# Optimization experiments

Hardware: AMD Instinct MI355X
Metric: run time of the kernel (lower is better)

## Reference

```python
import jax, jax.numpy as jnp
import numpy as np
from jax import lax

B0, C0, H0, W0 = 4, 128, 48, 48
GR = 32  # growth rate
NL = 4   # dense layers


def conv1x1(x, w, b):
    # w: [O, Cin], x: [B, Cin, H, W]
    return jnp.einsum('oc,bchw->bohw', w, x) + b[None, :, None, None]


def conv3x3(x, w, b):
    y = lax.conv_general_dilated(x, w, (1, 1), [(1, 1), (1, 1)],
                                 dimension_numbers=('NCHW', 'OIHW', 'NCHW'))
    return y + b[None, :, None, None]


def batchnorm(x, g, b, eps=1e-5):
    # training-mode BatchNorm2d: batch statistics over (B, H, W)
    mu = jnp.mean(x, axis=(0, 2, 3), keepdims=True)
    var = jnp.var(x, axis=(0, 2, 3), keepdims=True)
    return (x - mu) * lax.rsqrt(var + eps) * g[None, :, None, None] + b[None, :, None, None]


def apply_rope(x):
    B, C, H, W = x.shape
    half = C // 2
    theta = 1.0 / (10000.0 ** (jnp.arange(half, dtype=x.dtype) / half))
    # pos_emb[h, w, j] = (h + w) * theta[j]
    pos = (jnp.arange(H, dtype=x.dtype)[:, None, None]
           + jnp.arange(W, dtype=x.dtype)[None, :, None]) * theta
    cos = jnp.cos(pos).transpose(2, 0, 1)  # [half, H, W]
    sin = jnp.sin(pos).transpose(2, 0, 1)
    xr = x.reshape(B, half, 2, H, W)
    x_re, x_im = xr[:, :, 0], xr[:, :, 1]
    rr = x_re * cos - x_im * sin
    ri = x_re * sin + x_im * cos
    return jnp.stack([rr, ri], axis=2).reshape(B, C, H, W)


def setup_inputs() -> dict:
    key = jax.random.key(0)
    ks = iter(jax.random.split(key, 64))
    def nrm(shape, s=0.05):
        return jax.random.normal(next(ks), shape, jnp.float32) * s
    C = C0
    dc = C + NL * GR  # 256 dense-block output channels
    hid = 4 * C
    d = {
        'x': jax.random.normal(next(ks), (B0, C0, H0, W0), jnp.float32),
        'r_w': nrm((C, C)), 'r_b': jnp.zeros((C,), jnp.float32),
        'k_w': nrm((C, C)), 'k_b': jnp.zeros((C,), jnp.float32),
        'v_w': nrm((C, C)), 'v_b': jnp.zeros((C,), jnp.float32),
        'wc1_w': nrm((C // 4, C, 3, 3)), 'wc1_b': jnp.zeros((C // 4,), jnp.float32),
        'wc2_w': nrm((C, C // 4)), 'wc2_b': jnp.zeros((C,), jnp.float32),
        'u': nrm((C,), 0.1),
        'sn1_w': nrm((dc // 4, dc)), 'sn1_b': jnp.zeros((dc // 4,), jnp.float32),
        'sn2_w': nrm((dc, dc // 4)), 'sn2_b': jnp.zeros((dc,), jnp.float32),
        'lb_w': nrm((C // 4, dc)), 'lb_b': jnp.zeros((C // 4,), jnp.float32),
        'ld_w': nrm((C // 4, dc)), 'ld_b': jnp.zeros((C // 4,), jnp.float32),
        'ps_w': nrm((C, C // 4)), 'ps_b': jnp.zeros((C,), jnp.float32),
        'pq_w': nrm((C, C)), 'pq_b': jnp.zeros((C,), jnp.float32),
        'fc1_w': nrm((hid, C)), 'fc1_b': jnp.zeros((hid,), jnp.float32),
        'fc2_w': nrm((C, hid)), 'fc2_b': jnp.zeros((C,), jnp.float32),
    }
    for i in range(NL):
        cin = C + i * GR
        d[f'db_g{i}'] = jnp.ones((cin,), jnp.float32)
        d[f'db_b{i}'] = jnp.zeros((cin,), jnp.float32)
        d[f'db_w{i}'] = nrm((GR, cin, 3, 3))
        d[f'db_cb{i}'] = jnp.zeros((GR,), jnp.float32)
    return d


def _forward(x, r_w, r_b, k_w, k_b, v_w, v_b, wc1_w, wc1_b, wc2_w, wc2_b, u,
             db_g0, db_b0, db_w0, db_cb0, db_g1, db_b1, db_w1, db_cb1,
             db_g2, db_b2, db_w2, db_cb2, db_g3, db_b3, db_w3, db_cb3,
             sn1_w, sn1_b, sn2_w, sn2_b, lb_w, lb_b, ld_w, ld_b,
             ps_w, ps_b, pq_w, pq_b, fc1_w, fc1_b, fc2_w, fc2_b):
    B, C, H, W = x.shape
    N = H * W
    # decay gate w (hidden is None so it multiplies zeros, kept for fidelity)
    w_gate = jax.nn.sigmoid(conv1x1(jax.nn.relu(conv3x3(x, wc1_w, wc1_b)), wc2_w, wc2_b)).reshape(B, C, N)
    x_rope = apply_rope(x)
    r = jax.nn.sigmoid(conv1x1(x, r_w, r_b))
    k = conv1x1(x_rope, k_w, k_b).reshape(B, C, N)
    v = conv1x1(x_rope, v_w, v_b).reshape(B, C, N)
    zeros = jnp.zeros_like(k)
    new_num = zeros * jnp.exp(-w_gate) + k * v
    new_den = zeros * jnp.exp(-w_gate) + k
    eu = jnp.exp(u)[None, :, None]
    wkv = ((new_num + eu * k * v) / (new_den + eu * k)).reshape(B, C, H, W)
    recursive_output = r * wkv
    # dense block (concat-growth)
    feats = x
    for g, bb, wt, cb in ((db_g0, db_b0, db_w0, db_cb0), (db_g1, db_b1, db_w1, db_cb1),
                          (db_g2, db_b2, db_w2, db_cb2), (db_g3, db_b3, db_w3, db_cb3)):
        h = jax.nn.relu(batchnorm(feats, g, bb))
        feats = jnp.concatenate([feats, conv3x3(h, wt, cb)], axis=1)
    df = feats  # [B, C+4*GR, H, W]
    # adaptive spiking neuron
    tau = jnp.mean(jax.nn.sigmoid(conv1x1(jax.nn.relu(conv1x1(df, sn1_w, sn1_b)), sn2_w, sn2_b)),
                   axis=(2, 3), keepdims=True)
    spike_prob = jax.nn.sigmoid((df - 1.0) * 5.0)
    sf = spike_prob * (df * jnp.exp(-1.0 / (tau + 1e-6))) + (1.0 - spike_prob) * df
    # first attention over N tokens, channels = C//4
    Bf = conv1x1(sf, lb_w, lb_b).reshape(B, -1, N)
    Df = conv1x1(sf, ld_w, ld_b).reshape(B, -1, N)
    attn = jax.nn.softmax(jnp.einsum('bcn,bcm->bnm', Bf, Bf), axis=-1)
    att1 = jnp.einsum('bnm,bcm->bcn', attn, Df).reshape(B, -1, H, W)
    spike_output = conv1x1(att1, ps_w, ps_b)
    combined = recursive_output + spike_output
    # second attention (k/v convs are shared with WKV path)
    Q = conv1x1(combined, pq_w, pq_b).reshape(B, C, N)
    K = conv1x1(combined, k_w, k_b).reshape(B, C, N)
    V = conv1x1(combined, v_w, v_b).reshape(B, C, N)
    scores = jnp.einsum('bcn,bcm->bnm', Q, K) / jnp.sqrt(jnp.asarray(C, x.dtype))
    aw = jax.nn.softmax(scores, axis=-1)
    att2 = jnp.einsum('bnm,bcm->bcn', aw, V).reshape(B, C, H, W)
    x1 = x + att2
    out = x1 + conv1x1(jax.nn.relu(conv1x1(x1, fc1_w, fc1_b)) ** 2, fc2_w, fc2_b)
    return out, new_num, new_den


def reference(x, r_w, r_b, k_w, k_b, v_w, v_b, wc1_w, wc1_b, wc2_w, wc2_b, u,
              db_g0, db_b0, db_w0, db_cb0, db_g1, db_b1, db_w1, db_cb1,
              db_g2, db_b2, db_w2, db_cb2, db_g3, db_b3, db_w3, db_cb3,
              sn1_w, sn1_b, sn2_w, sn2_b, lb_w, lb_b, ld_w, ld_b,
              ps_w, ps_b, pq_w, pq_b, fc1_w, fc1_b, fc2_w, fc2_b):
    return _forward(x, r_w, r_b, k_w, k_b, v_w, v_b, wc1_w, wc1_b, wc2_w, wc2_b, u,
                    db_g0, db_b0, db_w0, db_cb0, db_g1, db_b1, db_w1, db_cb1,
                    db_g2, db_b2, db_w2, db_cb2, db_g3, db_b3, db_w3, db_cb3,
                    sn1_w, sn1_b, sn2_w, sn2_b, lb_w, lb_b, ld_w, ld_b,
                    ps_w, ps_b, pq_w, pq_b, fc1_w, fc1_b, fc2_w, fc2_b)
```

## Files before the change

kernel.cpp:

```cpp
#include <hip/hip_runtime.h>
#include <math.h>

#define BB 4
#define CC 128
#define HH 48
#define WW 48
#define NSP (HH*WW)
#define DCC 256
#define BCN (BB*CC*NSP)
#define KS 4

typedef float f32x4 __attribute__((ext_vector_type(4)));
typedef __bf16 bf16x8 __attribute__((ext_vector_type(8)));
typedef __bf16 bf16x4 __attribute__((ext_vector_type(4)));

__device__ __forceinline__ float sigmf(float v) { return 1.0f / (1.0f + __expf(-v)); }

struct Prep {
  const float* wsrc[13];
  int wlen[13];
  int woff[13];
  const float* psrc[4];
  int pcin[4];
  int poff[4];
  const float* x;
  float* sums;
  float* sums2;
  __bf16* x_t;
  __bf16* xrope_t;
};
__global__ __launch_bounds__(256) void prep_kernel(Prep a, __bf16* __restrict__ wdst,
                                                   __bf16* __restrict__ pdst) {
  __shared__ float lds[32][33];
  __shared__ float rs[4], rs2[4];
  int g = blockIdx.y;
  int idx = blockIdx.x * 256 + threadIdx.x;
  if (g < 13) {
    if (idx < a.wlen[g]) wdst[a.woff[g] + idx] = (__bf16)a.wsrc[g][idx];
  } else if (g < 17) {
    int L = g - 13;
    int cin = a.pcin[L];
    if (idx < 9 * 32 * cin) {
      int c = idx % cin;
      int o = (idx / cin) % 32;
      int tap = idx / (cin * 32);
      pdst[a.poff[L] + idx] = (__bf16)a.psrc[L][((size_t)o * cin + c) * 9 + tap];
    }
  } else if (g == 17) {
    int c = blockIdx.x;
    if (c >= 128) return;
    float s = 0.f, s2 = 0.f;
    for (int i = threadIdx.x; i < BB * NSP; i += 256) {
      int b = i / NSP, n = i % NSP;
      float v = a.x[((size_t)b * 128 + c) * NSP + n];
      s += v;
      s2 += v * v;
    }
#pragma unroll
    for (int off = 32; off > 0; off >>= 1) {
      s += __shfl_down(s, off);
      s2 += __shfl_down(s2, off);
    }
    int wid = threadIdx.x >> 6;
    if ((threadIdx.x & 63) == 0) { rs[wid] = s; rs2[wid] = s2; }
    __syncthreads();
    if (threadIdx.x == 0) {
      a.sums[c] = rs[0] + rs[1] + rs[2] + rs[3];
      a.sums2[c] = rs2[0] + rs2[1] + rs2[2] + rs2[3];
    }
  } else {
    int T = (g - 18) * 256 + blockIdx.x;
    if (T >= 1152) return;
    int b = T / 288;
    int r = T % 288;
    int c0 = (r / 72) * 32;
    int n0 = (r % 72) * 32;
    int tid = threadIdx.x;
    int nn = tid & 31, cs = tid >> 5;
#pragma unroll
    for (int j = 0; j < 4; ++j) {
      int cc = c0 + cs * 4 + j;
      lds[cs * 4 + j][nn] = a.x[((size_t)b * 128 + cc) * NSP + n0 + nn];
    }
    __syncthreads();
    int c = tid & 31, ns = tid >> 5;
#pragma unroll
    for (int j = 0; j < 4; ++j) {
      int n2 = ns * 4 + j;
      float pv = lds[c][n2];
      a.x_t[((size_t)b * NSP + n0 + n2) * 128 + c0 + c] = (__bf16)pv;
      int gc = c0 + c;
      int i = gc >> 1;
      float re = lds[c & ~1][n2];
      float im = lds[c | 1][n2];
      int n = n0 + n2;
      int h = n / WW, w = n % WW;
      float theta = __expf(-9.2103403719761836f * ((float)i) / 64.0f);
      float pos = (float)(h + w) * theta;
      float cs_ = cosf(pos), sn_ = sinf(pos);
      float vr_ = (gc & 1) ? (re * sn_ + im * cs_) : (re * cs_ - im * sn_);
      a.xrope_t[((size_t)b * NSP + n0 + n2) * 128 + c0 + c] = (__bf16)vr_;
    }
  }
}

__global__ __launch_bounds__(256) void kvr_kernel(
    const __bf16* __restrict__ xrope_t, const __bf16* __restrict__ x_t,
    const __bf16* __restrict__ wk, const __bf16* __restrict__ wvp,
    const __bf16* __restrict__ wr,
    const float* __restrict__ k_b, const float* __restrict__ v_b,
    const float* __restrict__ r_b, const float* __restrict__ u,
    float* __restrict__ kden, float* __restrict__ knum, float* __restrict__ rec) {
  int tid = threadIdx.x;
  int wv = tid >> 6, lane = tid & 63;
  int m15 = lane & 15, quad = lane >> 4;
  int b = blockIdx.y;
  int n0 = blockIdx.x * 16;
  int o0 = wv * 32;
  int n = n0 + m15;
  const __bf16* brr = xrope_t + ((size_t)b * NSP + n) * 128 + quad * 8;
  const __bf16* brx = x_t + ((size_t)b * NSP + n) * 128 + quad * 8;
  const __bf16* ak0 = wk + (size_t)(o0 + m15) * 128 + quad * 8;
  const __bf16* ak1 = wk + (size_t)(o0 + 16 + m15) * 128 + quad * 8;
  const __bf16* av0 = wvp + (size_t)(o0 + m15) * 128 + quad * 8;
  const __bf16* av1 = wvp + (size_t)(o0 + 16 + m15) * 128 + quad * 8;
  const __bf16* ar0 = wr + (size_t)(o0 + m15) * 128 + quad * 8;
  const __bf16* ar1 = wr + (size_t)(o0 + 16 + m15) * 128 + quad * 8;
  f32x4 fk[2], fv[2], fr[2];
#pragma unroll
  for (int t = 0; t < 2; ++t) {
    fk[t] = (f32x4){0.f, 0.f, 0.f, 0.f};
    fv[t] = (f32x4){0.f, 0.f, 0.f, 0.f};
    fr[t] = (f32x4){0.f, 0.f, 0.f, 0.f};
  }
#pragma unroll
  for (int kc = 0; kc < 128; kc += 32) {
    bf16x8 br_ = *(const bf16x8*)(brr + kc);
    bf16x8 bx_ = *(const bf16x8*)(brx + kc);
    fk[0] = __builtin_amdgcn_mfma_f32_16x16x32_bf16(*(const bf16x8*)(ak0 + kc), br_, fk[0], 0, 0, 0);
    fk[1] = __builtin_amdgcn_mfma_f32_16x16x32_bf16(*(const bf16x8*)(ak1 + kc), br_, fk[1], 0, 0, 0);
    fv[0] = __builtin_amdgcn_mfma_f32_16x16x32_bf16(*(const bf16x8*)(av0 + kc), br_, fv[0], 0, 0, 0);
    fv[1] = __builtin_amdgcn_mfma_f32_16x16x32_bf16(*(const bf16x8*)(av1 + kc), br_, fv[1], 0, 0, 0);
    fr[0] = __builtin_amdgcn_mfma_f32_16x16x32_bf16(*(const bf16x8*)(ar0 + kc), bx_, fr[0], 0, 0, 0);
    fr[1] = __builtin_amdgcn_mfma_f32_16x16x32_bf16(*(const bf16x8*)(ar1 + kc), bx_, fr[1], 0, 0, 0);
  }
#pragma unroll
  for (int t = 0; t < 2; ++t) {
#pragma unroll
    for (int reg = 0; reg < 4; ++reg) {
      int ol = o0 + t * 16 + quad * 4 + reg;
      float kk = fk[t][reg] + k_b[ol];
      float vv = fv[t][reg] + v_b[ol];
      float rr = sigmf(fr[t][reg] + r_b[ol]);
      float eu = __expf(u[ol]);
      size_t idx = ((size_t)b * 128 + ol) * NSP + n;
      float nv = kk * vv, tt = eu * kk;
      kden[idx] = kk;
      knum[idx] = nv;
      rec[idx] = rr * ((nv + tt * vv) / (kk + tt));
    }
  }
}

template <int OUT>
__device__ __forceinline__ void gemm_store(void* outp, int b, int n, int Oseg,
                                           int obase, int quad, const float* vr) {
  if (OUT == 0) {
    float* op = (float*)outp;
#pragma unroll
    for (int reg = 0; reg < 4; ++reg)
      op[((size_t)b * Oseg + obase + quad * 4 + reg) * NSP + n] = vr[reg];
  } else if (OUT == 1) {
    __bf16* op = (__bf16*)outp;
    bf16x4 pk;
#pragma unroll
    for (int reg = 0; reg < 4; ++reg) pk[reg] = (__bf16)vr[reg];
    *(bf16x4*)(op + ((size_t)b * NSP + n) * Oseg + obase + quad * 4) = pk;
  } else {
    __bf16* op = (__bf16*)outp;
#pragma unroll
    for (int reg = 0; reg < 4; ++reg)
      op[((size_t)b * Oseg + obase + quad * 4 + reg) * NSP + n] = (__bf16)vr[reg];
  }
}

template <int K, int ACT, int OUT0, int OUT1, int OUT2, int SPLITB>
__global__ __launch_bounds__(256) void gemm_mfma_kernel(
    const __bf16* __restrict__ in_t, const __bf16* __restrict__ in_t2,
    const __bf16* __restrict__ wb,
    const float* __restrict__ bias0, const float* __restrict__ bias1,
    const float* __restrict__ bias2,
    const float* __restrict__ add0, const float* __restrict__ add1,
    void* __restrict__ out0, void* __restrict__ out1, void* __restrict__ out2,
    int osplit, int osplit2, int Ototal, float sc0, float sc1, float sc2) {
  int tid = threadIdx.x;
  int wv = tid >> 6, lane = tid & 63;
  int m15 = lane & 15, quad = lane >> 4;
  int b = blockIdx.y;
  int n0 = blockIdx.x * 16;
  int wpb = blockDim.x >> 6;
  int o0 = (blockIdx.z * wpb + wv) * 32;
  if (o0 >= Ototal) return;
  int n = n0 + m15;
  const __bf16* brow = in_t + ((size_t)b * NSP + n) * (SPLITB ? 128 : K) + quad * 8;
  const __bf16* brow2 = SPLITB ? (in_t2 + ((size_t)b * NSP + n) * 128 + quad * 8) : nullptr;
  const __bf16* a0p = wb + (size_t)(o0 + m15) * K + quad * 8;
  const __bf16* a1p = wb + (size_t)(o0 + 16 + m15) * K + quad * 8;
  f32x4 of0 = (f32x4){0.f, 0.f, 0.f, 0.f};
  f32x4 of1 = (f32x4){0.f, 0.f, 0.f, 0.f};
#pragma unroll
  for (int kc = 0; kc < K; kc += 32) {
    bf16x8 bfr;
    if constexpr (SPLITB) {
      bfr = (kc < 128) ? *(const bf16x8*)(brow + kc) : *(const bf16x8*)(brow2 + (kc - 128));
    } else {
      bfr = *(const bf16x8*)(brow + kc);
    }
    bf16x8 a0 = *(const bf16x8*)(a0p + kc);
    bf16x8 a1 = *(const bf16x8*)(a1p + kc);
    of0 = __builtin_amdgcn_mfma_f32_16x16x32_bf16(a0, bfr, of0, 0, 0, 0);
    of1 = __builtin_amdgcn_mfma_f32_16x16x32_bf16(a1, bfr, of1, 0, 0, 0);
  }
  int seg = (o0 >= osplit2) ? 2 : (o0 >= osplit) ? 1 : 0;
  int segb = (seg == 2) ? osplit2 : (seg == 1) ? osplit : 0;
  int sege = (seg == 2) ? Ototal : (seg == 1) ? osplit2 : osplit;
  int Oseg = sege - segb;
  int ol0 = o0 - segb;
  const float* bias = (seg == 2) ? bias2 : (seg == 1) ? bias1 : bias0;
  const float* add = (seg == 2) ? nullptr : (seg == 1) ? add1 : add0;
  void* outp = (seg == 2) ? out2 : (seg == 1) ? out1 : out0;
  float sc = (seg == 2) ? sc2 : (seg == 1) ? sc1 : sc0;
#pragma unroll
  for (int t = 0; t < 2; ++t) {
    f32x4 acc = t ? of1 : of0;
    float vr[4];
#pragma unroll
    for (int reg = 0; reg < 4; ++reg) {
      int ol = ol0 + t * 16 + quad * 4 + reg;
      float v = acc[reg] + bias[ol];
      if (ACT == 1) v = fmaxf(v, 0.0f);
      else if (ACT == 2) v = sigmf(v);
      else if (ACT == 3) { v = fmaxf(v, 0.0f); v = v * v; }
      v *= sc;
      if (add) v += add[((size_t)b * Oseg + ol) * NSP + n];
      vr[reg] = v;
    }
    if (seg == 0) gemm_store<OUT0>(outp, b, n, Oseg, ol0 + t * 16, quad, vr);
    else if (seg == 1) gemm_store<OUT1>(outp, b, n, Oseg, ol0 + t * 16, quad, vr);
    else gemm_store<OUT2>(outp, b, n, Oseg, ol0 + t * 16, quad, vr);
  }
}

__global__ __launch_bounds__(256) void sn12_kernel(
    const __bf16* __restrict__ x_t, const __bf16* __restrict__ dense_t,
    const __bf16* __restrict__ wsn1, const float* __restrict__ sn1_b,
    const __bf16* __restrict__ wsn2, const float* __restrict__ sn2_b,
    float* __restrict__ taupart) {
  __shared__ __bf16 z1l[16][72];
  int tid = threadIdx.x;
  int wv = tid >> 6, lane = tid & 63;
  int m15 = lane & 15, quad = lane >> 4;
  int b = blockIdx.y;
  int n0 = blockIdx.x * 16;
  int n = n0 + m15;
  if (wv < 2) {
    int o0 = wv * 32;
    const __bf16* bx = x_t + ((size_t)b * NSP + n) * 128 + quad * 8;
    const __bf16* bd = dense_t + ((size_t)b * NSP + n) * 128 + quad * 8;
    const __bf16* a0p = wsn1 + (size_t)(o0 + m15) * 256 + quad * 8;
    const __bf16* a1p = wsn1 + (size_t)(o0 + 16 + m15) * 256 + quad * 8;
    f32x4 of0 = (f32x4){0.f, 0.f, 0.f, 0.f};
    f32x4 of1 = (f32x4){0.f, 0.f, 0.f, 0.f};
#pragma unroll
    for (int kc = 0; kc < 256; kc += 32) {
      bf16x8 bfr = (kc < 128) ? *(const bf16x8*)(bx + kc) : *(const bf16x8*)(bd + (kc - 128));
      bf16x8 a0 = *(const bf16x8*)(a0p + kc);
      bf16x8 a1 = *(const bf16x8*)(a1p + kc);
      of0 = __builtin_amdgcn_mfma_f32_16x16x32_bf16(a0, bfr, of0, 0, 0, 0);
      of1 = __builtin_amdgcn_mfma_f32_16x16x32_bf16(a1, bfr, of1, 0, 0, 0);
    }
#pragma unroll
    for (int t = 0; t < 2; ++t) {
      f32x4 acc = t ? of1 : of0;
#pragma unroll
      for (int reg = 0; reg < 4; ++reg) {
        int ol = o0 + t * 16 + quad * 4 + reg;
        z1l[m15][ol] = (__bf16)fmaxf(acc[reg] + sn1_b[ol], 0.0f);
      }
    }
  }
  __syncthreads();
  bf16x8 bfr0 = *(const bf16x8*)&z1l[m15][quad * 8];
  bf16x8 bfr1 = *(const bf16x8*)&z1l[m15][32 + quad * 8];
#pragma unroll
  for (int ot = 0; ot < 2; ++ot) {
    int o0 = (wv * 2 + ot) * 32;
    const __bf16* a0p = wsn2 + (size_t)(o0 + m15) * 64 + quad * 8;
    const __bf16* a1p = wsn2 + (size_t)(o0 + 16 + m15) * 64 + quad * 8;
    f32x4 of0 = (f32x4){0.f, 0.f, 0.f, 0.f};
    f32x4 of1 = (f32x4){0.f, 0.f, 0.f, 0.f};
    of0 = __builtin_amdgcn_mfma_f32_16x16x32_bf16(*(const bf16x8*)(a0p), bfr0, of0, 0, 0, 0);
    of0 = __builtin_amdgcn_mfma_f32_16x16x32_bf16(*(const bf16x8*)(a0p + 32), bfr1, of0, 0, 0, 0);
    of1 = __builtin_amdgcn_mfma_f32_16x16x32_bf16(*(const bf16x8*)(a1p), bfr0, of1, 0, 0, 0);
    of1 = __builtin_amdgcn_mfma_f32_16x16x32_bf16(*(const bf16x8*)(a1p + 32), bfr1, of1, 0, 0, 0);
#pragma unroll
    for (int t = 0; t < 2; ++t) {
      f32x4 acc = t ? of1 : of0;
#pragma unroll
      for (int reg = 0; reg < 4; ++reg) {
        int ol = o0 + t * 16 + quad * 4 + reg;
        float sv = sigmf(acc[reg] + sn2_b[ol]);
        sv += __shfl_xor(sv, 1);
        sv += __shfl_xor(sv, 2);
        sv += __shfl_xor(sv, 4);
        sv += __shfl_xor(sv, 8);
        if (m15 == 0)
          taupart[((size_t)(b * DCC + ol)) * 144 + blockIdx.x] = sv;
      }
    }
  }
}

__global__ __launch_bounds__(128) void lbld_sf_kernel(
    const __bf16* __restrict__ x_t, const __bf16* __restrict__ dense_t,
    const float* __restrict__ taupart, const __bf16* __restrict__ wlb,
    const float* __restrict__ lb_b, const float* __restrict__ ld_b,
    __bf16* __restrict__ Bft, __bf16* __restrict__ Dfb) {
  __shared__ float ef[256];
  int tid = threadIdx.x;
  int b = blockIdx.y;
  for (int ch = tid; ch < 256; ch += 128) {
    const f32x4* tp = (const f32x4*)(taupart + ((size_t)(b * DCC + ch)) * 144);
    f32x4 s4 = (f32x4){0.f, 0.f, 0.f, 0.f};
#pragma unroll
    for (int j = 0; j < 36; ++j) s4 += tp[j];
    float tv = (s4.x + s4.y + s4.z + s4.w) * (1.0f / (float)NSP);
    ef[ch] = __expf(-1.0f / (tv + 1e-6f)) - 1.0f;
  }
  __syncthreads();
  int wv = tid >> 6, lane = tid & 63;
  int m15 = lane & 15, quad = lane >> 4;
  int n0 = blockIdx.x * 16;
  int o0 = wv * 32;
  int n = n0 + m15;
  const __bf16* bx = x_t + ((size_t)b * NSP + n) * 128 + quad * 8;
  const __bf16* bd = dense_t + ((size_t)b * NSP + n) * 128 + quad * 8;
  const __bf16* a0p = wlb + (size_t)(o0 + m15) * 256 + quad * 8;
  const __bf16* a1p = wlb + (size_t)(o0 + 16 + m15) * 256 + quad * 8;
  f32x4 of0 = (f32x4){0.f, 0.f, 0.f, 0.f};
  f32x4 of1 = (f32x4){0.f, 0.f, 0.f, 0.f};
#pragma unroll
  for (int kc = 0; kc < 256; kc += 32) {
    bf16x8 raw = (kc < 128) ? *(const bf16x8*)(bx + kc) : *(const bf16x8*)(bd + (kc - 128));
    bf16x8 sfv;
#pragma unroll
    for (int j = 0; j < 8; ++j) {
      float df = (float)raw[j];
      float sp = sigmf((df - 1.0f) * 5.0f);
      sfv[j] = (__bf16)(df * (1.0f + sp * ef[kc + quad * 8 + j]));
    }
    bf16x8 a0 = *(const bf16x8*)(a0p + kc);
    bf16x8 a1 = *(const bf16x8*)(a1p + kc);
    of0 = __builtin_amdgcn_mfma_f32_16x16x32_bf16(a0, sfv, of0, 0, 0, 0);
    of1 = __builtin_amdgcn_mfma_f32_16x16x32_bf16(a1, sfv, of1, 0, 0, 0);
  }
  if (o0 == 0) {
#pragma unroll
    for (int t = 0; t < 2; ++t) {
      f32x4 acc = t ? of1 : of0;
      bf16x4 pk;
#pragma unroll
      for (int reg = 0; reg < 4; ++reg) pk[reg] = (__bf16)(acc[reg] + lb_b[t * 16 + quad * 4 + reg]);
      *(bf16x4*)(Bft + ((size_t)b * NSP + n) * 32 + t * 16 + quad * 4) = pk;
    }
  } else {
#pragma unroll
    for (int t = 0; t < 2; ++t) {
      f32x4 acc = t ? of1 : of0;
#pragma unroll
      for (int reg = 0; reg < 4; ++reg) {
        int ol = t * 16 + quad * 4 + reg;
        Dfb[((size_t)b * 32 + ol) * NSP + n] = (__bf16)(acc[reg] + ld_b[ol]);
      }
    }
  }
}

template <int Cin>
__global__ __launch_bounds__(256) void convbn_kernel(
    const __bf16* __restrict__ x_t, const __bf16* __restrict__ dense_t,
    const __bf16* __restrict__ wb, const float* __restrict__ cb,
    float* __restrict__ sums, float* __restrict__ sums2,
    const float* __restrict__ cpart_in,
    const float* __restrict__ g, const float* __restrict__ bbp,
    __bf16* __restrict__ dense_out, float* __restrict__ cpart_out, int cout0) {
  constexpr int KCin = Cin / 32;
  constexpr int NIT = 9 * KCin;
  __shared__ float red[4][64][8];
  __shared__ float scsh[2][Cin];
  __shared__ float tred[64][4];
  __shared__ float fin[64];
  int tid = threadIdx.x;
  const float inv = 1.0f / (float)(BB * NSP);

  if (cpart_in) {
    int row = tid >> 2, sl = tid & 3;
    const f32x4* cp = (const f32x4*)(cpart_in + (size_t)row * 576 + sl * 144);
    f32x4 s4 = (f32x4){0.f, 0.f, 0.f, 0.f};
#pragma unroll
    for (int j = 0; j < 36; ++j) s4 += cp[j];
    tred[row][sl] = s4.x + s4.y + s4.z + s4.w;
    __syncthreads();
    if (tid < 64) fin[tid] = tred[tid][0] + tred[tid][1] + tred[tid][2] + tred[tid][3];
    __syncthreads();
    if (blockIdx.x == 0 && blockIdx.y == 0 && tid < 32) {
      sums[Cin - 32 + tid] = fin[tid];
      sums2[Cin - 32 + tid] = fin[32 + tid];
    }
  }
  for (int ch = tid; ch < Cin; ch += 256) {
    float S, S2;
    if (cpart_in && ch >= Cin - 32) {
      S = fin[ch - (Cin - 32)];
      S2 = fin[ch - (Cin - 32) + 32];
    } else {
      S = sums[ch];
      S2 = sums2[ch];
    }
    float m = S * inv;
    float var = S2 * inv - m * m;
    float sc_ = rsqrtf(var + 1e-5f) * g[ch];
    scsh[0][ch] = sc_;
    scsh[1][ch] = bbp[ch] - m * sc_;
  }
  __syncthreads();

  int wv = tid >> 6, lane = tid & 63;
  int m15 = lane & 15, quad = lane >> 4;
  int b = blockIdx.y;
  int n0 = blockIdx.x * 16;
  int n = n0 + m15;
  int h = n / WW, w = n % WW;
  f32x4 of0 = (f32x4){0.f, 0.f, 0.f, 0.f};
  f32x4 of1 = (f32x4){0.f, 0.f, 0.f, 0.f};
  const __bf16* bx_ = x_t + (size_t)b * NSP * 128;
  const __bf16* bd_ = dense_t + (size_t)b * NSP * 128;
  const bf16x8 zf = {};
  int begin = (wv * NIT) / 4, end = ((wv + 1) * NIT) / 4;
  int cur = -1;
  float bsc[8], bsh[8];
  const __bf16* base = nullptr;
  for (int ci = begin; ci < end; ++ci) {
    int chunk = ci / 9;
    int tap = ci - chunk * 9;
    int kc = chunk * 32;
    if (chunk != cur) {
      cur = chunk;
      int cc = kc + quad * 8;
#pragma unroll
      for (int j = 0; j < 8; ++j) {
        bsc[j] = scsh[0][cc + j];
        bsh[j] = scsh[1][cc + j];
      }
      base = (cc < 128) ? (bx_ + cc) : (bd_ + cc - 128);
    }
    int dh = tap / 3 - 1, dw = tap % 3 - 1;
    bool valid = ((unsigned)(h + dh) < HH) && ((unsigned)(w + dw) < WW);
    int pa = valid ? (n + dh * WW + dw) : 0;
    bf16x8 raw = *(const bf16x8*)(base + (size_t)pa * 128);
    bf16x8 bfr;
#pragma unroll
    for (int j = 0; j < 8; ++j) {
      float v = fmaxf((float)raw[j] * bsc[j] + bsh[j], 0.0f);
      bfr[j] = (__bf16)v;
    }
    if (!valid) bfr = zf;
    const __bf16* wt = wb + (size_t)tap * 32 * Cin + kc + quad * 8;
    bf16x8 a0 = *(const bf16x8*)(wt + (size_t)m15 * Cin);
    bf16x8 a1 = *(const bf16x8*)(wt + (size_t)(16 + m15) * Cin);
    of0 = __builtin_amdgcn_mfma_f32_16x16x32_bf16(a0, bfr, of0, 0, 0, 0);
    of1 = __builtin_amdgcn_mfma_f32_16x16x32_bf16(a1, bfr, of1, 0, 0, 0);
  }
  float* myred = red[wv][lane];
#pragma unroll
  for (int reg = 0; reg < 4; ++reg) {
    myred[reg] = of0[reg];
    myred[4 + reg] = of1[reg];
  }
  __syncthreads();
  if (wv == 0) {
    int dloc = cout0 - 128;
    __bf16* dt = dense_out + ((size_t)b * NSP + n) * 128 + dloc;
    bf16x4 pk0, pk1;
    float sv[4][4];
#pragma unroll
    for (int reg = 0; reg < 4; ++reg) {
      int o = quad * 4 + reg;
      float v0 = red[0][lane][reg] + red[1][lane][reg] + red[2][lane][reg] +
                 red[3][lane][reg] + cb[o];
      float v1 = red[0][lane][4 + reg] + red[1][lane][4 + reg] + red[2][lane][4 + reg] +
                 red[3][lane][4 + reg] + cb[16 + o];
      pk0[reg] = (__bf16)v0;
      pk1[reg] = (__bf16)v1;
      sv[reg][0] = v0;
      sv[reg][1] = v0 * v0;
      sv[reg][2] = v1;
      sv[reg][3] = v1 * v1;
    }
    *(bf16x4*)(dt + quad * 4) = pk0;
    *(bf16x4*)(dt + 16 + quad * 4) = pk1;
    if (cpart_out) {
#pragma unroll
      for (int reg = 0; reg < 4; ++reg) {
        float a0 = sv[reg][0], q0 = sv[reg][1], a1 = sv[reg][2], q1 = sv[reg][3];
#pragma unroll
        for (int mk = 1; mk < 16; mk <<= 1) {
          a0 += __shfl_xor(a0, mk);
          q0 += __shfl_xor(q0, mk);
          a1 += __shfl_xor(a1, mk);
          q1 += __shfl_xor(q1, mk);
        }
        if (m15 == 0) {
          int o = quad * 4 + reg;
          int pidx = blockIdx.y * 144 + blockIdx.x;
          cpart_out[(size_t)o * 576 + pidx] = a0;
          cpart_out[(size_t)(32 + o) * 576 + pidx] = q0;
          cpart_out[(size_t)(16 + o) * 576 + pidx] = a1;
          cpart_out[(size_t)(48 + o) * 576 + pidx] = q1;
        }
      }
    }
  }
}

template <int CD>
__global__ __launch_bounds__(256) void attn_part_kernel(
    const __bf16* __restrict__ Qt, const __bf16* __restrict__ Kt,
    const __bf16* __restrict__ Vb, __bf16* __restrict__ Op,
    float* __restrict__ lp) {
  constexpr int NC = CD / 16;
  constexpr int KC = CD / 32;
  constexpr int KEYS = NSP / KS;
  constexpr int KP = CD + 4;
  constexpr int VP = 36;
  __shared__ __bf16 kl[32][KP];
  __shared__ __bf16 vl[CD][VP];
  int tid = threadIdx.x;
  int wv = tid >> 6, lane = tid & 63;
  int m15 = lane & 15, quad = lane >> 4;
  int b = blockIdx.y, ks = blockIdx.z;
  int n0 = blockIdx.x * 64 + wv * 16;

  bf16x8 qf[KC];
  const __bf16* qrow = Qt + ((size_t)b * NSP + n0 + m15) * CD + quad * 8;
#pragma unroll
  for (int kc = 0; kc < KC; ++kc) qf[kc] = *(const bf16x8*)(qrow + kc * 32);

  f32x4 of[NC];
#pragma unroll
  for (int i = 0; i < NC; ++i) of[i] = (f32x4){0.f, 0.f, 0.f, 0.f};
  float lsum = 0.f;

  const __bf16* Kb = Kt + (size_t)b * NSP * CD;
  const __bf16* Vbb = Vb + (size_t)b * CD * NSP;

  for (int m0 = ks * KEYS; m0 < (ks + 1) * KEYS; m0 += 32) {
    __syncthreads();
    for (int i = tid; i < 32 * CD / 8; i += 256) {
      int row = i / (CD / 8);
      int cc8 = (i % (CD / 8)) * 8;
      *(bf16x8*)&kl[row][cc8] = *(const bf16x8*)(Kb + (size_t)(m0 + row) * CD + cc8);
    }
    for (int i = tid; i < CD * 4; i += 256) {
      int ch = i / 4;
      int k8 = (i % 4) * 8;
      *(bf16x8*)&vl[ch][k8] = *(const bf16x8*)(Vbb + (size_t)ch * NSP + m0 + k8);
    }
    __syncthreads();
    f32x4 s[2];
#pragma unroll
    for (int t = 0; t < 2; ++t) {
      f32x4 acc = (f32x4){0.f, 0.f, 0.f, 0.f};
#pragma unroll
      for (int kc = 0; kc < KC; ++kc) {
        bf16x8 kf = *(const bf16x8*)&kl[t * 16 + m15][kc * 32 + quad * 8];
        acc = __builtin_amdgcn_mfma_f32_16x16x32_bf16(kf, qf[kc], acc, 0, 0, 0);
      }
      s[t] = acc;
    }
    bf16x8 pf;
#pragma unroll
    for (int t = 0; t < 2; ++t) {
#pragma unroll
      for (int r = 0; r < 4; ++r) {
        float ev = __expf(s[t][r]);
        lsum += ev;
        pf[t * 4 + r] = (__bf16)ev;
      }
    }
#pragma unroll
    for (int ct = 0; ct < NC; ++ct) {
      bf16x4 va = *(const bf16x4*)&vl[ct * 16 + m15][4 * quad];
      bf16x4 vb_ = *(const bf16x4*)&vl[ct * 16 + m15][16 + 4 * quad];
      bf16x8 vf;
#pragma unroll
      for (int j = 0; j < 4; ++j) { vf[j] = va[j]; vf[4 + j] = vb_[j]; }
      of[ct] = __builtin_amdgcn_mfma_f32_16x16x32_bf16(pf, vf, of[ct], 0, 0, 0);
    }
  }

  lsum += __shfl_xor(lsum, 16);
  lsum += __shfl_xor(lsum, 32);
  float* lpb = lp + (size_t)(ks * BB + b) * NSP + n0;
  if (quad == 0) lpb[m15] = lsum;
  __bf16* Ob = Op + (size_t)(ks * BB + b) * CD * NSP;
#pragma unroll
  for (int ct = 0; ct < NC; ++ct) {
    bf16x4 pk;
#pragma unroll
    for (int reg = 0; reg < 4; ++reg) pk[reg] = (__bf16)of[ct][reg];
    *(bf16x4*)(Ob + (size_t)(ct * 16 + m15) * NSP + n0 + quad * 4) = pk;
  }
}

__global__ __launch_bounds__(256) void c32ps_kernel(
    const __bf16* __restrict__ Op, const float* __restrict__ lp,
    const __bf16* __restrict__ wps, const float* __restrict__ ps_b,
    const float* __restrict__ rec, __bf16* __restrict__ comb_t) {
  __shared__ float lds[32][33];
  int b = blockIdx.y;
  int n0 = blockIdx.x * 32;
  int tid = threadIdx.x;
  int nn = tid & 31, cs = tid >> 5;
  float ltot = 0.f;
#pragma unroll
  for (int ks = 0; ks < KS; ++ks) ltot += lp[(size_t)(ks * BB + b) * NSP + n0 + nn];
  float linv = 1.0f / ltot;
#pragma unroll
  for (int j = 0; j < 4; ++j) {
    int cc = cs * 4 + j;
    float s = 0.f;
#pragma unroll
    for (int ks = 0; ks < KS; ++ks)
      s += (float)Op[((size_t)(ks * BB + b) * 32 + cc) * NSP + n0 + nn];
    lds[cc][nn] = s * linv;
  }
  __syncthreads();
  int wv = tid >> 6, lane = tid & 63;
  int m15 = lane & 15, quad = lane >> 4;
  int o0 = wv * 32;
  bf16x8 a0 = *(const bf16x8*)(wps + (size_t)(o0 + m15) * 32 + quad * 8);
  bf16x8 a1 = *(const bf16x8*)(wps + (size_t)(o0 + 16 + m15) * 32 + quad * 8);
#pragma unroll
  for (int t2 = 0; t2 < 2; ++t2) {
    int nl = t2 * 16 + m15;
    int n = n0 + nl;
    bf16x8 bfr;
#pragma unroll
    for (int j = 0; j < 8; ++j) bfr[j] = (__bf16)lds[quad * 8 + j][nl];
    f32x4 of0 = (f32x4){0.f, 0.f, 0.f, 0.f};
    f32x4 of1 = (f32x4){0.f, 0.f, 0.f, 0.f};
    of0 = __builtin_amdgcn_mfma_f32_16x16x32_bf16(a0, bfr, of0, 0, 0, 0);
    of1 = __builtin_amdgcn_mfma_f32_16x16x32_bf16(a1, bfr, of1, 0, 0, 0);
#pragma unroll
    for (int t = 0; t < 2; ++t) {
      f32x4 acc = t ? of1 : of0;
      bf16x4 pk;
#pragma unroll
      for (int reg = 0; reg < 4; ++reg) {
        int ol = o0 + t * 16 + quad * 4 + reg;
        float v = acc[reg] + ps_b[ol] + rec[((size_t)b * 128 + ol) * NSP + n];
        pk[reg] = (__bf16)v;
      }
      *(bf16x4*)(comb_t + ((size_t)b * NSP + n) * 128 + o0 + t * 16 + quad * 4) = pk;
    }
  }
}

__global__ __launch_bounds__(256) void combine128_kernel(
    const __bf16* __restrict__ Op, const float* __restrict__ lp,
    const float* __restrict__ x, float* __restrict__ x1, __bf16* __restrict__ x1_t) {
  __shared__ float lds[32][33];
  int b = blockIdx.z;
  int n0 = blockIdx.x * 32;
  int c0 = blockIdx.y * 32;
  int tid = threadIdx.x;
  int nn = tid & 31, cs = tid >> 5;
  float ltot = 0.f;
#pragma unroll
  for (int ks = 0; ks < KS; ++ks) ltot += lp[(size_t)(ks * BB + b) * NSP + n0 + nn];
  float linv = 1.0f / ltot;
#pragma unroll
  for (int j = 0; j < 4; ++j) {
    int gc = c0 + cs * 4 + j;
    float s = 0.f;
#pragma unroll
    for (int ks = 0; ks < KS; ++ks)
      s += (float)Op[((size_t)(ks * BB + b) * CC + gc) * NSP + n0 + nn];
    float v = s * linv + x[((size_t)b * CC + gc) * NSP + n0 + nn];
    lds[cs * 4 + j][nn] = v;
    x1[((size_t)b * CC + gc) * NSP + n0 + nn] = v;
  }
  __syncthreads();
  int c = tid & 31, ns = tid >> 5;
#pragma unroll
  for (int j = 0; j < 4; ++j) {
    int n2 = ns * 4 + j;
    x1_t[((size_t)b * NSP + n0 + n2) * CC + c0 + c] = (__bf16)lds[c][n2];
  }
}

extern "C" void kernel_launch(void* const* d_in, const int* in_sizes, int n_in,
                              void* d_out, int out_size, void* d_ws, size_t ws_size,
                              hipStream_t stream) {
  const float* x = (const float*)d_in[0];
  const float* r_w = (const float*)d_in[1];
  const float* r_b = (const float*)d_in[2];
  const float* k_w = (const float*)d_in[3];
  const float* k_b = (const float*)d_in[4];
  const float* v_w = (const float*)d_in[5];
  const float* v_b = (const float*)d_in[6];
  const float* u = (const float*)d_in[11];
  const float* sn1_w = (const float*)d_in[12];
  const float* sn1_b = (const float*)d_in[13];
  const float* sn2_w = (const float*)d_in[14];
  const float* sn2_b = (const float*)d_in[15];
  const float* lb_w = (const float*)d_in[16];
  const float* lb_b = (const float*)d_in[17];
  const float* ld_w = (const float*)d_in[18];
  const float* ld_b = (const float*)d_in[19];
  const float* ps_w = (const float*)d_in[20];
  const float* ps_b = (const float*)d_in[21];
  const float* pq_w = (const float*)d_in[22];
  const float* pq_b = (const float*)d_in[23];
  const float* fc1_w = (const float*)d_in[24];
  const float* fc1_b = (const float*)d_in[25];
  const float* fc2_w = (const float*)d_in[26];
  const float* fc2_b = (const float*)d_in[27];
  const float* db_g[4] = {(const float*)d_in[28], (const float*)d_in[32],
                          (const float*)d_in[36], (const float*)d_in[40]};
  const float* db_b[4] = {(const float*)d_in[29], (const float*)d_in[33],
                          (const float*)d_in[37], (const float*)d_in[41]};
  const float* db_w[4] = {(const float*)d_in[30], (const float*)d_in[34],
                          (const float*)d_in[38], (const float*)d_in[42]};
  const float* db_cb[4] = {(const float*)d_in[31], (const float*)d_in[35],
                           (const float*)d_in[39], (const float*)d_in[43]};

  float* outp = (float*)d_out;
  float* knum = outp + BCN;
  float* kden = outp + 2 * (size_t)BCN;

  float* ws = (float*)d_ws;
  const size_t F_FEATS = 0;
  const size_t F_REC = 4718592;
  const size_t F_V = 5898240;
  const size_t F_R = 7077888;
  const size_t F_XR = 8257536;
  const size_t F_XT = 8847360;
  const size_t F_DFB = 9437184;
  const size_t F_AT1T = 9584640;
  const size_t F_CT = 9732096;
  const size_t F_LP = 10321920;
  const size_t F_WB = 10434048;
  const size_t F_WB3 = 10575360;
  const size_t F_STATS = 10676736;
  const size_t F_TAUP = 10714112;
  float* sums = ws + F_STATS;
  float* sums2 = ws + F_STATS + 256;
  float* cpart0 = ws + F_FEATS;
  float* cpart1 = cpart0 + 36864;
  float* cpart2 = cpart1 + 36864;
  float* taupart = ws + F_TAUP;
  float* lp = ws + F_LP;
  __bf16* wbase = (__bf16*)(ws + F_WB);
  __bf16* wb3 = (__bf16*)(ws + F_WB3);
  const int W_KV = 0;
  const int W_R = 32768;
  const int W_SN1 = 49152;
  const int W_SN2 = 65536;
  const int W_LBLD = 81920;
  const int W_PS = 98304;
  const int W_PQK = 102400;
  const int W_FC1 = 151552;
  const int W_FC2 = 217088;
  const int W3_OFF[4] = {0, 36864, 82944, 138240};

  dim3 blk(256);
  __bf16* xrope_t = (__bf16*)(ws + F_XR);
  __bf16* x_t = (__bf16*)(ws + F_XT);

  Prep pp;
  pp.wsrc[0] = k_w;    pp.wlen[0] = 16384; pp.woff[0] = W_KV;
  pp.wsrc[1] = v_w;    pp.wlen[1] = 16384; pp.woff[1] = W_KV + 16384;
  pp.wsrc[2] = r_w;    pp.wlen[2] = 16384; pp.woff[2] = W_R;
  pp.wsrc[3] = sn1_w;  pp.wlen[3] = 16384; pp.woff[3] = W_SN1;
  pp.wsrc[4] = sn2_w;  pp.wlen[4] = 16384; pp.woff[4] = W_SN2;
  pp.wsrc[5] = lb_w;   pp.wlen[5] = 8192;  pp.woff[5] = W_LBLD;
  pp.wsrc[6] = ld_w;   pp.wlen[6] = 8192;  pp.woff[6] = W_LBLD + 8192;
  pp.wsrc[7] = ps_w;   pp.wlen[7] = 4096;  pp.woff[7] = W_PS;
  pp.wsrc[8] = pq_w;   pp.wlen[8] = 16384; pp.woff[8] = W_PQK;
  pp.wsrc[9] = k_w;    pp.wlen[9] = 16384; pp.woff[9] = W_PQK + 16384;
  pp.wsrc[10] = v_w;   pp.wlen[10] = 16384; pp.woff[10] = W_PQK + 32768;
  pp.wsrc[11] = fc1_w; pp.wlen[11] = 65536; pp.woff[11] = W_FC1;
  pp.wsrc[12] = fc2_w; pp.wlen[12] = 65536; pp.woff[12] = W_FC2;
  for (int i = 0; i < 4; ++i) {
    pp.psrc[i] = db_w[i];
    pp.pcin[i] = 128 + 32 * i;
    pp.poff[i] = W3_OFF[i];
  }
  pp.x = x;
  pp.sums = sums;
  pp.sums2 = sums2;
  pp.x_t = x_t;
  pp.xrope_t = xrope_t;
  prep_kernel<<<dim3(256, 23), blk, 0, stream>>>(pp, wbase, wb3);

  kvr_kernel<<<dim3(144, 4), blk, 0, stream>>>(
      xrope_t, x_t, wbase + W_KV, wbase + W_KV + 16384, wbase + W_R,
      k_b, v_b, r_b, u, kden, knum, ws + F_REC);

  __bf16* dense_t = (__bf16*)(ws + F_R);
  convbn_kernel<128><<<dim3(144, 4), blk, 0, stream>>>(
      x_t, dense_t, wb3 + W3_OFF[0], db_cb[0], sums, sums2, nullptr,
      db_g[0], db_b[0], dense_t, cpart0, 128);
  convbn_kernel<160><<<dim3(144, 4), blk, 0, stream>>>(
      x_t, dense_t, wb3 + W3_OFF[1], db_cb[1], sums, sums2, cpart0,
      db_g[1], db_b[1], dense_t, cpart1, 160);
  convbn_kernel<192><<<dim3(144, 4), blk, 0, stream>>>(
      x_t, dense_t, wb3 + W3_OFF[2], db_cb[2], sums, sums2, cpart1,
      db_g[2], db_b[2], dense_t, cpart2, 192);
  convbn_kernel<224><<<dim3(144, 4), blk, 0, stream>>>(
      x_t, dense_t, wb3 + W3_OFF[3], db_cb[3], sums, sums2, cpart2,
      db_g[3], db_b[3], dense_t, nullptr, 224);

  sn12_kernel<<<dim3(144, 4), blk, 0, stream>>>(
      x_t, dense_t, wbase + W_SN1, sn1_b, wbase + W_SN2, sn2_b, taupart);
  __bf16* Bft = (__bf16*)(ws + F_CT + 294912);
  __bf16* Dfb = (__bf16*)(ws + F_DFB);
  lbld_sf_kernel<<<dim3(144, 4), dim3(128), 0, stream>>>(
      x_t, dense_t, taupart, wbase + W_LBLD, lb_b, ld_b, Bft, Dfb);
  __bf16* Opart = (__bf16*)(ws + F_FEATS);
  attn_part_kernel<32><<<dim3(36, 4, KS), blk, 0, stream>>>(Bft, Bft, Dfb, Opart, lp);
  __bf16* comb_t = (__bf16*)(ws + F_CT);
  c32ps_kernel<<<dim3(72, 4), blk, 0, stream>>>(
      Opart, lp, wbase + W_PS, ps_b, ws + F_REC, comb_t);

  __bf16* Qt = (__bf16*)(ws + F_XR);
  __bf16* K2t = (__bf16*)(ws + F_XT);
  __bf16* V2b = (__bf16*)(ws + F_V);
  gemm_mfma_kernel<128, 0, 1, 1, 2, 0><<<dim3(144, 4, 3), blk, 0, stream>>>(
      comb_t, nullptr, wbase + W_PQK, pq_b, k_b, v_b, nullptr, nullptr,
      Qt, K2t, V2b, 128, 256, 384, 0.08838834764831845f, 1.f, 1.f);
  attn_part_kernel<128><<<dim3(36, 4, KS), blk, 0, stream>>>(Qt, K2t, V2b, Opart, lp);
  float* x1 = ws + F_R;
  __bf16* x1_t = (__bf16*)(ws + F_CT);
  combine128_kernel<<<dim3(72, 4, 4), blk, 0, stream>>>(Opart, lp, x, x1, x1_t);

  __bf16* h_t = (__bf16*)(ws + F_FEATS);
  gemm_mfma_kernel<128, 3, 1, 1, 0, 0><<<dim3(144, 4, 4), blk, 0, stream>>>(
      x1_t, nullptr, wbase + W_FC1, fc1_b, fc1_b, nullptr, nullptr, nullptr,
      h_t, h_t, nullptr, 512, 512, 512, 1.f, 1.f, 1.f);
  gemm_mfma_kernel<512, 0, 0, 0, 0, 0><<<dim3(144, 4, 1), blk, 0, stream>>>(
      h_t, nullptr, wbase + W_FC2, fc2_b, fc2_b, nullptr, x1, x1,
      outp, outp, nullptr, 128, 128, 128, 1.f, 1.f, 1.f);
}
```

Before: 405.5 us.

## Fuse projection-sum with QKV GEMM and FC1/FC2 MLP into single kernels

```diff
diff --git a/kernel.cpp b/kernel.cpp
--- a/kernel.cpp
+++ b/kernel.cpp
@@ -162,95 +162,6 @@
   }
 }
 
-template <int OUT>
-__device__ __forceinline__ void gemm_store(void* outp, int b, int n, int Oseg,
-                                           int obase, int quad, const float* vr) {
-  if (OUT == 0) {
-    float* op = (float*)outp;
-#pragma unroll
-    for (int reg = 0; reg < 4; ++reg)
-      op[((size_t)b * Oseg + obase + quad * 4 + reg) * NSP + n] = vr[reg];
-  } else if (OUT == 1) {
-    __bf16* op = (__bf16*)outp;
-    bf16x4 pk;
-#pragma unroll
-    for (int reg = 0; reg < 4; ++reg) pk[reg] = (__bf16)vr[reg];
-    *(bf16x4*)(op + ((size_t)b * NSP + n) * Oseg + obase + quad * 4) = pk;
-  } else {
-    __bf16* op = (__bf16*)outp;
-#pragma unroll
-    for (int reg = 0; reg < 4; ++reg)
-      op[((size_t)b * Oseg + obase + quad * 4 + reg) * NSP + n] = (__bf16)vr[reg];
-  }
-}
-
-template <int K, int ACT, int OUT0, int OUT1, int OUT2, int SPLITB>
-__global__ __launch_bounds__(256) void gemm_mfma_kernel(
-    const __bf16* __restrict__ in_t, const __bf16* __restrict__ in_t2,
-    const __bf16* __restrict__ wb,
-    const float* __restrict__ bias0, const float* __restrict__ bias1,
-    const float* __restrict__ bias2,
-    const float* __restrict__ add0, const float* __restrict__ add1,
-    void* __restrict__ out0, void* __restrict__ out1, void* __restrict__ out2,
-    int osplit, int osplit2, int Ototal, float sc0, float sc1, float sc2) {
-  int tid = threadIdx.x;
-  int wv = tid >> 6, lane = tid & 63;
-  int m15 = lane & 15, quad = lane >> 4;
-  int b = blockIdx.y;
-  int n0 = blockIdx.x * 16;
-  int wpb = blockDim.x >> 6;
-  int o0 = (blockIdx.z * wpb + wv) * 32;
-  if (o0 >= Ototal) return;
-  int n = n0 + m15;
-  const __bf16* brow = in_t + ((size_t)b * NSP + n) * (SPLITB ? 128 : K) + quad * 8;
-  const __bf16* brow2 = SPLITB ? (in_t2 + ((size_t)b * NSP + n) * 128 + quad * 8) : nullptr;
-  const __bf16* a0p = wb + (size_t)(o0 + m15) * K + quad * 8;
-  const __bf16* a1p = wb + (size_t)(o0 + 16 + m15) * K + quad * 8;
-  f32x4 of0 = (f32x4){0.f, 0.f, 0.f, 0.f};
-  f32x4 of1 = (f32x4){0.f, 0.f, 0.f, 0.f};
-#pragma unroll
-  for (int kc = 0; kc < K; kc += 32) {
-    bf16x8 bfr;
-    if constexpr (SPLITB) {
-      bfr = (kc < 128) ? *(const bf16x8*)(brow + kc) : *(const bf16x8*)(brow2 + (kc - 128));
-    } else {
-      bfr = *(const bf16x8*)(brow + kc);
-    }
-    bf16x8 a0 = *(const bf16x8*)(a0p + kc);
-    bf16x8 a1 = *(const bf16x8*)(a1p + kc);
-    of0 = __builtin_amdgcn_mfma_f32_16x16x32_bf16(a0, bfr, of0, 0, 0, 0);
-    of1 = __builtin_amdgcn_mfma_f32_16x16x32_bf16(a1, bfr, of1, 0, 0, 0);
-  }
-  int seg = (o0 >= osplit2) ? 2 : (o0 >= osplit) ? 1 : 0;
-  int segb = (seg == 2) ? osplit2 : (seg == 1) ? osplit : 0;
-  int sege = (seg == 2) ? Ototal : (seg == 1) ? osplit2 : osplit;
-  int Oseg = sege - segb;
-  int ol0 = o0 - segb;
-  const float* bias = (seg == 2) ? bias2 : (seg == 1) ? bias1 : bias0;
-  const float* add = (seg == 2) ? nullptr : (seg == 1) ? add1 : add0;
-  void* outp = (seg == 2) ? out2 : (seg == 1) ? out1 : out0;
-  float sc = (seg == 2) ? sc2 : (seg == 1) ? sc1 : sc0;
-#pragma unroll
-  for (int t = 0; t < 2; ++t) {
-    f32x4 acc = t ? of1 : of0;
-    float vr[4];
-#pragma unroll
-    for (int reg = 0; reg < 4; ++reg) {
-      int ol = ol0 + t * 16 + quad * 4 + reg;
-      float v = acc[reg] + bias[ol];
-      if (ACT == 1) v = fmaxf(v, 0.0f);
-      else if (ACT == 2) v = sigmf(v);
-      else if (ACT == 3) { v = fmaxf(v, 0.0f); v = v * v; }
-      v *= sc;
-      if (add) v += add[((size_t)b * Oseg + ol) * NSP + n];
-      vr[reg] = v;
-    }
-    if (seg == 0) gemm_store<OUT0>(outp, b, n, Oseg, ol0 + t * 16, quad, vr);
-    else if (seg == 1) gemm_store<OUT1>(outp, b, n, Oseg, ol0 + t * 16, quad, vr);
-    else gemm_store<OUT2>(outp, b, n, Oseg, ol0 + t * 16, quad, vr);
-  }
-}
-
 __global__ __launch_bounds__(256) void sn12_kernel(
     const __bf16* __restrict__ x_t, const __bf16* __restrict__ dense_t,
     const __bf16* __restrict__ wsn1, const float* __restrict__ sn1_b,
@@ -623,11 +534,15 @@
   }
 }
 
-__global__ __launch_bounds__(256) void c32ps_kernel(
+__global__ __launch_bounds__(256) void c32psqkv_kernel(
     const __bf16* __restrict__ Op, const float* __restrict__ lp,
     const __bf16* __restrict__ wps, const float* __restrict__ ps_b,
-    const float* __restrict__ rec, __bf16* __restrict__ comb_t) {
+    const float* __restrict__ rec, const __bf16* __restrict__ wpqk,
+    const float* __restrict__ pq_b, const float* __restrict__ k_b,
+    const float* __restrict__ v_b, __bf16* __restrict__ Qt,
+    __bf16* __restrict__ K2t, __bf16* __restrict__ V2b, float qscale) {
   __shared__ float lds[32][33];
+  __shared__ __bf16 comb[32][136];
   int b = blockIdx.y;
   int n0 = blockIdx.x * 32;
   int tid = threadIdx.x;
@@ -672,7 +587,52 @@
         float v = acc[reg] + ps_b[ol] + rec[((size_t)b * 128 + ol) * NSP + n];
         pk[reg] = (__bf16)v;
       }
-      *(bf16x4*)(comb_t + ((size_t)b * NSP + n) * 128 + o0 + t * 16 + quad * 4) = pk;
+      *(bf16x4*)&comb[nl][o0 + t * 16 + quad * 4] = pk;
+    }
+  }
+  __syncthreads();
+#pragma unroll
+  for (int j = 0; j < 3; ++j) {
+    int og = (wv * 3 + j) * 32;
+    int seg = og >> 7;
+    int ol0 = og & 127;
+    const __bf16* a0p = wpqk + (size_t)(og + m15) * 128 + quad * 8;
+    const __bf16* a1p = wpqk + (size_t)(og + 16 + m15) * 128 + quad * 8;
+#pragma unroll
+    for (int t2 = 0; t2 < 2; ++t2) {
+      int nl = t2 * 16 + m15;
+      int n = n0 + nl;
+      f32x4 of0 = (f32x4){0.f, 0.f, 0.f, 0.f};
+      f32x4 of1 = (f32x4){0.f, 0.f, 0.f, 0.f};
+#pragma unroll
+      for (int kc = 0; kc < 128; kc += 32) {
+        bf16x8 bfr = *(const bf16x8*)&comb[nl][kc + quad * 8];
+        of0 = __builtin_amdgcn_mfma_f32_16x16x32_bf16(*(const bf16x8*)(a0p + kc), bfr, of0, 0, 0, 0);
+        of1 = __builtin_amdgcn_mfma_f32_16x16x32_bf16(*(const bf16x8*)(a1p + kc), bfr, of1, 0, 0, 0);
+      }
+#pragma unroll
+      for (int t = 0; t < 2; ++t) {
+        f32x4 acc = t ? of1 : of0;
+        if (seg == 0) {
+          bf16x4 pk;
+#pragma unroll
+          for (int reg = 0; reg < 4; ++reg)
+            pk[reg] = (__bf16)((acc[reg] + pq_b[ol0 + t * 16 + quad * 4 + reg]) * qscale);
+          *(bf16x4*)(Qt + ((size_t)b * NSP + n) * 128 + ol0 + t * 16 + quad * 4) = pk;
+        } else if (seg == 1) {
+          bf16x4 pk;
+#pragma unroll
+          for (int reg = 0; reg < 4; ++reg)
+            pk[reg] = (__bf16)(acc[reg] + k_b[ol0 + t * 16 + quad * 4 + reg]);
+          *(bf16x4*)(K2t + ((size_t)b * NSP + n) * 128 + ol0 + t * 16 + quad * 4) = pk;
+        } else {
+#pragma unroll
+          for (int reg = 0; reg < 4; ++reg) {
+            int ol = ol0 + t * 16 + quad * 4 + reg;
+            V2b[((size_t)b * 128 + ol) * NSP + n] = (__bf16)(acc[reg] + v_b[ol]);
+          }
+        }
+      }
     }
   }
 }
@@ -707,6 +667,70 @@
   for (int j = 0; j < 4; ++j) {
     int n2 = ns * 4 + j;
     x1_t[((size_t)b * NSP + n0 + n2) * CC + c0 + c] = (__bf16)lds[c][n2];
+  }
+}
+
+__global__ __launch_bounds__(256) void fc12_kernel(
+    const __bf16* __restrict__ x1_t, const __bf16* __restrict__ wfc1,
+    const float* __restrict__ fc1_b, const __bf16* __restrict__ wfc2,
+    const float* __restrict__ fc2_b, const float* __restrict__ x1,
+    float* __restrict__ outp) {
+  __shared__ __bf16 hl[16][520];
+  int tid = threadIdx.x;
+  int wv = tid >> 6, lane = tid & 63;
+  int m15 = lane & 15, quad = lane >> 4;
+  int b = blockIdx.y;
+  int n0 = blockIdx.x * 16;
+  int n = n0 + m15;
+  const __bf16* brow = x1_t + ((size_t)b * NSP + n) * 128 + quad * 8;
+  bf16x8 bf[4];
+#pragma unroll
+  for (int kc = 0; kc < 4; ++kc) bf[kc] = *(const bf16x8*)(brow + kc * 32);
+#pragma unroll
+  for (int j = 0; j < 4; ++j) {
+    int o0 = (wv * 4 + j) * 32;
+    const __bf16* a0p = wfc1 + (size_t)(o0 + m15) * 128 + quad * 8;
+    const __bf16* a1p = wfc1 + (size_t)(o0 + 16 + m15) * 128 + quad * 8;
+    f32x4 of0 = (f32x4){0.f, 0.f, 0.f, 0.f};
+    f32x4 of1 = (f32x4){0.f, 0.f, 0.f, 0.f};
+#pragma unroll
+    for (int kc = 0; kc < 4; ++kc) {
+      of0 = __builtin_amdgcn_mfma_f32_16x16x32_bf16(*(const bf16x8*)(a0p + kc * 32), bf[kc], of0, 0, 0, 0);
+      of1 = __builtin_amdgcn_mfma_f32_16x16x32_bf16(*(const bf16x8*)(a1p + kc * 32), bf[kc], of1, 0, 0, 0);
+    }
+#pragma unroll
+    for (int t = 0; t < 2; ++t) {
+      f32x4 acc = t ? of1 : of0;
+      bf16x4 pk;
+#pragma unroll
+      for (int reg = 0; reg < 4; ++reg) {
+        float v = fmaxf(acc[reg] + fc1_b[o0 + t * 16 + quad * 4 + reg], 0.0f);
+        pk[reg] = (__bf16)(v * v);
+      }
+      *(bf16x4*)&hl[m15][o0 + t * 16 + quad * 4] = pk;
+    }
+  }
+  __syncthreads();
+  int o0 = wv * 32;
+  const __bf16* a0p = wfc2 + (size_t)(o0 + m15) * 512 + quad * 8;
+  const __bf16* a1p = wfc2 + (size_t)(o0 + 16 + m15) * 512 + quad * 8;
+  f32x4 of0 = (f32x4){0.f, 0.f, 0.f, 0.f};
+  f32x4 of1 = (f32x4){0.f, 0.f, 0.f, 0.f};
+#pragma unroll
+  for (int kc = 0; kc < 512; kc += 32) {
+    bf16x8 bfr = *(const bf16x8*)&hl[m15][kc + quad * 8];
+    of0 = __builtin_amdgcn_mfma_f32_16x16x32_bf16(*(const bf16x8*)(a0p + kc), bfr, of0, 0, 0, 0);
+    of1 = __builtin_amdgcn_mfma_f32_16x16x32_bf16(*(const bf16x8*)(a1p + kc), bfr, of1, 0, 0, 0);
+  }
+#pragma unroll
+  for (int t = 0; t < 2; ++t) {
+    f32x4 acc = t ? of1 : of0;
+#pragma unroll
+    for (int reg = 0; reg < 4; ++reg) {
+      int ol = o0 + t * 16 + quad * 4 + reg;
+      size_t idx = ((size_t)b * 128 + ol) * NSP + n;
+      outp[idx] = acc[reg] + fc2_b[ol] + x1[idx];
+    }
   }
 }
 
@@ -758,7 +782,6 @@
   const size_t F_XR = 8257536;
   const size_t F_XT = 8847360;
   const size_t F_DFB = 9437184;
-  const size_t F_AT1T = 9584640;
   const size_t F_CT = 9732096;
   const size_t F_LP = 10321920;
   const size_t F_WB = 10434048;
@@ -841,26 +864,19 @@
       x_t, dense_t, taupart, wbase + W_LBLD, lb_b, ld_b, Bft, Dfb);
   __bf16* Opart = (__bf16*)(ws + F_FEATS);
   attn_part_kernel<32><<<dim3(36, 4, KS), blk, 0, stream>>>(Bft, Bft, Dfb, Opart, lp);
-  __bf16* comb_t = (__bf16*)(ws + F_CT);
-  c32ps_kernel<<<dim3(72, 4), blk, 0, stream>>>(
-      Opart, lp, wbase + W_PS, ps_b, ws + F_REC, comb_t);
 
   __bf16* Qt = (__bf16*)(ws + F_XR);
   __bf16* K2t = (__bf16*)(ws + F_XT);
   __bf16* V2b = (__bf16*)(ws + F_V);
-  gemm_mfma_kernel<128, 0, 1, 1, 2, 0><<<dim3(144, 4, 3), blk, 0, stream>>>(
-      comb_t, nullptr, wbase + W_PQK, pq_b, k_b, v_b, nullptr, nullptr,
-      Qt, K2t, V2b, 128, 256, 384, 0.08838834764831845f, 1.f, 1.f);
+  c32psqkv_kernel<<<dim3(72, 4), blk, 0, stream>>>(
+      Opart, lp, wbase + W_PS, ps_b, ws + F_REC, wbase + W_PQK,
+      pq_b, k_b, v_b, Qt, K2t, V2b, 0.08838834764831845f);
+
   attn_part_kernel<128><<<dim3(36, 4, KS), blk, 0, stream>>>(Qt, K2t, V2b, Opart, lp);
   float* x1 = ws + F_R;
   __bf16* x1_t = (__bf16*)(ws + F_CT);
   combine128_kernel<<<dim3(72, 4, 4), blk, 0, stream>>>(Opart, lp, x, x1, x1_t);
 
-  __bf16* h_t = (__bf16*)(ws + F_FEATS);
-  gemm_mfma_kernel<128, 3, 1, 1, 0, 0><<<dim3(144, 4, 4), blk, 0, stream>>>(
-      x1_t, nullptr, wbase + W_FC1, fc1_b, fc1_b, nullptr, nullptr, nullptr,
-      h_t, h_t, nullptr, 512, 512, 512, 1.f, 1.f, 1.f);
-  gemm_mfma_kernel<512, 0, 0, 0, 0, 0><<<dim3(144, 4, 1), blk, 0, stream>>>(
-      h_t, nullptr, wbase + W_FC2, fc2_b, fc2_b, nullptr, x1, x1,
-      outp, outp, nullptr, 128, 128, 128, 1.f, 1.f, 1.f);
-}
+  fc12_kernel<<<dim3(144, 4), blk, 0, stream>>>(
+      x1_t, wbase + W_FC1, fc1_b, wbase + W_FC2, fc2_b, x1, outp);
+}
```

After: 382.5 us. 5.7% less time.
